# Kernel tuning notes

Hardware: AMD Instinct MI355X
Metric: run time of the kernel (lower is better)

## Reference

```python
import jax, jax.numpy as jnp
import numpy as np

NEG_SLOPE = 0.01  # torch F.leaky_relu default


def _gat_stack(x, W, a1w, a1b, a2w, a2b):
    """One GAT stack over all heads.
    x: (B, N, F_in); W: (H, F_in, d); a1w/a2w: (H, d); a1b/a2b: (H,)
    returns (B, N, H*d) -- heads concatenated in order along last dim.
    """
    # 1x1 conv1d (no bias) == per-node linear projection
    fts = jnp.einsum('bnf,hfd->hbnd', x, W)                      # (H,B,N,d)
    f1 = jnp.einsum('hbnd,hd->hbn', fts, a1w) + a1b[:, None, None]
    f2 = jnp.einsum('hbnd,hd->hbn', fts, a2w) + a2b[:, None, None]
    # logits[h,b,i,j] = f1[h,b,i] + f2[h,b,j]  (f_1.permute + f_2 broadcast)
    logits = f1[:, :, :, None] + f2[:, :, None, :]               # (H,B,N,N)
    coefs = jax.nn.softmax(jax.nn.leaky_relu(logits, NEG_SLOPE), axis=-1)
    vals = jnp.einsum('hbnm,hbmd->hbnd', coefs, fts)             # bmm aggregation
    ret = jax.nn.elu(vals + fts)                                 # residual-within-head + ELU activation
    B, N = x.shape[0], x.shape[1]
    return jnp.transpose(ret, (1, 2, 0, 3)).reshape(B, N, -1)    # cat(heads, dim=-1)


def setup_inputs() -> dict:
    key = jax.random.key(0)
    ks = jax.random.split(key, 7)
    B, N, F_in, H, d = 32, 512, 128, 8, 64
    hidden = H * d  # 512
    s = 0.05
    return {
        'x':   jax.random.normal(ks[0], (B, N, F_in), jnp.float32),
        'W0':  jax.random.normal(ks[1], (H, F_in, d), jnp.float32) * s,
        'W1':  jax.random.normal(ks[2], (H, hidden, d), jnp.float32) * s,
        'a1w': jax.random.normal(ks[3], (2, H, d), jnp.float32) * s,
        'a1b': jax.random.normal(ks[4], (2, H), jnp.float32) * s,
        'a2w': jax.random.normal(ks[5], (2, H, d), jnp.float32) * s,
        'a2b': jax.random.normal(ks[6], (2, H), jnp.float32) * s,
    }


def reference(x, W0, W1, a1w, a1b, a2w, a2b):
    # stack 0: input dim = num_random_sample
    h = _gat_stack(x, W0, a1w[0], a1b[0], a2w[0], a2b[0])
    # stack 1: input dim = hidden_dim
    out = _gat_stack(h, W1, a1w[1], a1b[1], a2w[1], a2b[1])
    return out
```

## Files before the change

kernel.cpp:

```cpp
#include <hip/hip_runtime.h>
#include <hip/hip_bf16.h>
#include <stdint.h>

typedef __attribute__((ext_vector_type(8))) short short8;
typedef __attribute__((ext_vector_type(4))) float f32x4;

#define L2E 1.44269504f

__device__ __forceinline__ short f2bf(float f) {
    unsigned u = __builtin_bit_cast(unsigned, f);
    return (short)((u + 0x8000u) >> 16);
}
__device__ __forceinline__ float bf2f(short s) {
    unsigned u = ((unsigned)(unsigned short)s) << 16;
    return __builtin_bit_cast(float, u);
}

__global__ void wtrans_kernel(const float* __restrict__ W0, const float* __restrict__ W1,
                              short* __restrict__ BT0, short* __restrict__ BT1) {
    int idx = blockIdx.x * 256 + threadIdx.x;
    if (idx < 8 * 128 * 64) {
        int h = idx >> 13;
        int k = (idx >> 6) & 127;
        int dd = idx & 63;
        BT0[(h * 64 + dd) * 128 + k] = f2bf(W0[idx]);
    } else {
        int j = idx - 8 * 128 * 64;
        int h = j >> 15;
        int k = (j >> 6) & 511;
        int dd = j & 63;
        BT1[(h * 64 + dd) * 512 + k] = f2bf(W1[j]);
    }
}

template <typename AT>
__global__ __launch_bounds__(256, 2)
void gemm_kernel(const AT* __restrict__ A, const short* __restrict__ BT,
                 short* __restrict__ fts, int K) {
    __shared__ __align__(16) short As[128 * 40];
    __shared__ __align__(16) short Bs[128 * 40];

    const int tid  = threadIdx.x;
    const int lane = tid & 63;
    const int w    = tid >> 6;
    const int wr   = w >> 1, wc = w & 1;
    const int quad = lane >> 4, l15 = lane & 15;
    const int m0   = blockIdx.y * 128;
    const int n0   = blockIdx.x * 128;

    f32x4 acc[4][4];
    for (int i = 0; i < 4; ++i)
        for (int j = 0; j < 4; ++j) { f32x4 z = {0.f, 0.f, 0.f, 0.f}; acc[i][j] = z; }

    const int nkb = K >> 5;
    for (int kb = 0; kb < nkb; ++kb) {
        __syncthreads();
        if constexpr (sizeof(AT) == 4) {
            for (int i = 0; i < 4; ++i) {
                int id  = tid + i * 256;
                int row = id >> 3, kc = id & 7;
                float4 v = *(const float4*)((const float*)A + (size_t)(m0 + row) * K + kb * 32 + kc * 4);
                ushort4 p;
                p.x = (unsigned short)f2bf(v.x);
                p.y = (unsigned short)f2bf(v.y);
                p.z = (unsigned short)f2bf(v.z);
                p.w = (unsigned short)f2bf(v.w);
                *(ushort4*)(As + row * 40 + kc * 4) = p;
            }
        } else {
            for (int i = 0; i < 2; ++i) {
                int id  = tid + i * 256;
                int row = id >> 2, kc = id & 3;
                uint4 va = *(const uint4*)((const short*)A + (size_t)(m0 + row) * K + kb * 32 + kc * 8);
                *(uint4*)(As + row * 40 + kc * 8) = va;
            }
        }
        for (int i = 0; i < 2; ++i) {
            int id  = tid + i * 256;
            int row = id >> 2, kc = id & 3;
            uint4 vb = *(const uint4*)(BT + (size_t)(n0 + row) * K + kb * 32 + kc * 8);
            *(uint4*)(Bs + row * 40 + kc * 8) = vb;
        }
        __syncthreads();
        short8 af[4], bf[4];
        for (int mf = 0; mf < 4; ++mf)
            af[mf] = *(const short8*)(As + (wr * 64 + mf * 16 + l15) * 40 + quad * 8);
        for (int nf = 0; nf < 4; ++nf)
            bf[nf] = *(const short8*)(Bs + (wc * 64 + nf * 16 + l15) * 40 + quad * 8);
        for (int mf = 0; mf < 4; ++mf)
            for (int nf = 0; nf < 4; ++nf)
                acc[mf][nf] = __builtin_amdgcn_mfma_f32_16x16x32_bf16(af[mf], bf[nf], acc[mf][nf], 0, 0, 0);
    }

    for (int nf = 0; nf < 4; ++nf) {
        int col = n0 + wc * 64 + nf * 16 + l15;
        int h = col >> 6, dd = col & 63;
        for (int mf = 0; mf < 4; ++mf) {
            int m = m0 + wr * 64 + mf * 16 + quad * 4;
            int b = m >> 9, n = m & 511;
            ushort4 pk;
            pk.x = (unsigned short)f2bf(acc[mf][nf][0]);
            pk.y = (unsigned short)f2bf(acc[mf][nf][1]);
            pk.z = (unsigned short)f2bf(acc[mf][nf][2]);
            pk.w = (unsigned short)f2bf(acc[mf][nf][3]);
            *(ushort4*)(fts + (size_t)((h * 32 + b) * 64 + dd) * 512 + n) = pk;
        }
    }
}

template <typename OutT>
__global__ __launch_bounds__(256, 4)
void attn_kernel(const short* __restrict__ fts,
                 const float* __restrict__ a1w, const float* __restrict__ a1b,
                 const float* __restrict__ a2w, const float* __restrict__ a2b,
                 OutT* __restrict__ out) {
    __shared__ __align__(16) short fts_s[64 * 256];
    __shared__ float f1_s[128];
    __shared__ __align__(16) float f2_s[256];
    __shared__ __align__(16) float p2_s[256];
    __shared__ __align__(16) float q2_s[256];

    const int tid  = threadIdx.x;
    const int lane = tid & 63, w = tid >> 6;
    const int quad = lane >> 4, l15 = lane & 15;
    const int bx   = blockIdx.x;
    const int h    = bx >> 7;
    const int b    = (bx >> 2) & 31;
    const int quarter = bx & 3;
    const int r0   = quarter * 128;
    const int c0   = quarter >> 1;
    const size_t fbase = (size_t)((h * 32 + b) * 64) * 512;

    f32x4 acc[2][4];
    for (int i = 0; i < 2; ++i)
        for (int j = 0; j < 4; ++j) { f32x4 z = {0.f, 0.f, 0.f, 0.f}; acc[i][j] = z; }
    float Lp[2] = {0.f, 0.f};
    float f1r[2], P1r[2], Q1r[2];

    const float a1bf = a1b[h], a2bf = a2b[h];

    for (int ci = 0; ci < 2; ++ci) {
        const int c = (ci == 0) ? c0 : 1 - c0;
        __syncthreads();
        for (int i = 0; i < 8; ++i) {
            int id = tid + i * 256;
            int dd = id >> 5, nc = id & 31;
            uint4 v = *(const uint4*)(fts + fbase + dd * 512 + c * 256 + nc * 8);
            *(uint4*)(fts_s + dd * 256 + ((nc ^ (dd & 7)) << 3)) = v;
        }
        __syncthreads();
        {
            int j = tid;
            float s1 = 0.f, s2 = 0.f;
            for (int dd = 0; dd < 64; ++dd) {
                float v = bf2f(fts_s[dd * 256 + (((j >> 3) ^ (dd & 7)) << 3) + (j & 7)]);
                s1 += v * a1w[h * 64 + dd];
                s2 += v * a2w[h * 64 + dd];
            }
            float f2 = s2 + a2bf;
            f2_s[j] = f2;
            p2_s[j] = __builtin_amdgcn_exp2f(f2 * L2E);
            q2_s[j] = __builtin_amdgcn_exp2f(f2 * (0.01f * L2E));
            if (ci == 0) {
                int lo = r0 & 255;
                if (((unsigned)(j - lo)) < 128u) f1_s[j - lo] = s1 + a1bf;
            }
        }
        __syncthreads();
        if (ci == 0) {
            for (int rt = 0; rt < 2; ++rt) {
                float f1 = f1_s[w * 32 + rt * 16 + l15];
                f1r[rt] = f1;
                P1r[rt] = __builtin_amdgcn_exp2f(f1 * L2E);
                Q1r[rt] = __builtin_amdgcn_exp2f(f1 * (0.01f * L2E));
            }
        }
        for (int jb = 0; jb < 8; ++jb) {
            short8 bfr[4];
            for (int nf = 0; nf < 4; ++nf) {
                int col = nf * 16 + l15;
                bfr[nf] = *(const short8*)(fts_s + col * 256 + (((jb * 4 + quad) ^ (col & 7)) << 3));
            }
            int o = jb * 32 + quad * 8;
            f32x4 fa = *(const f32x4*)(f2_s + o), fb = *(const f32x4*)(f2_s + o + 4);
            f32x4 pa = *(const f32x4*)(p2_s + o), pb = *(const f32x4*)(p2_s + o + 4);
            f32x4 qa = *(const f32x4*)(q2_s + o), qb = *(const f32x4*)(q2_s + o + 4);
            float f2v[8] = {fa[0], fa[1], fa[2], fa[3], fb[0], fb[1], fb[2], fb[3]};
            float p2v[8] = {pa[0], pa[1], pa[2], pa[3], pb[0], pb[1], pb[2], pb[3]};
            float q2v[8] = {qa[0], qa[1], qa[2], qa[3], qb[0], qb[1], qb[2], qb[3]};

            for (int rt = 0; rt < 2; ++rt) {
                short8 ef;
                float lsum = 0.f;
                for (int t = 0; t < 8; ++t) {
                    float s = f1r[rt] + f2v[t];
                    float e = (s < 0.f) ? (Q1r[rt] * q2v[t]) : (P1r[rt] * p2v[t]);
                    lsum += e;
                    ef[t] = f2bf(e);
                }
                Lp[rt] += lsum;
                for (int nf = 0; nf < 4; ++nf)
                    acc[rt][nf] = __builtin_amdgcn_mfma_f32_16x16x32_bf16(ef, bfr[nf], acc[rt][nf], 0, 0, 0);
            }
        }
    }

    for (int rt = 0; rt < 2; ++rt) {
        float Lf = Lp[rt];
        Lf += __shfl_xor(Lf, 16, 64);
        Lf += __shfl_xor(Lf, 32, 64);
        float rinv[4];
        for (int r = 0; r < 4; ++r) {
            float Lr = __shfl(Lf, quad * 4 + r, 64);
            rinv[r] = __builtin_amdgcn_rcpf(Lr);
        }
        int i0 = r0 + w * 32 + rt * 16 + quad * 4;
        for (int nf = 0; nf < 4; ++nf) {
            int col = nf * 16 + l15;
            ushort4 res = *(const ushort4*)(fts + fbase + col * 512 + i0);
            unsigned short rr[4] = {res.x, res.y, res.z, res.w};
            for (int r = 0; r < 4; ++r) {
                float val = acc[rt][nf][r] * rinv[r] + bf2f((short)rr[r]);
                if (val < 0.f) val = __builtin_amdgcn_exp2f(val * L2E) - 1.f;
                size_t oidx = (size_t)(b * 512 + i0 + r) * 512 + h * 64 + col;
                if constexpr (sizeof(OutT) == 4) out[oidx] = val;
                else                             out[oidx] = f2bf(val);
            }
        }
    }
}

extern "C" void kernel_launch(void* const* d_in, const int* in_sizes, int n_in,
                              void* d_out, int out_size, void* d_ws, size_t ws_size,
                              hipStream_t stream) {
    const float* x   = (const float*)d_in[0];
    const float* W0  = (const float*)d_in[1];
    const float* W1  = (const float*)d_in[2];
    const float* a1w = (const float*)d_in[3];
    const float* a1b = (const float*)d_in[4];
    const float* a2w = (const float*)d_in[5];
    const float* a2b = (const float*)d_in[6];
    float* out = (float*)d_out;

    char* ws = (char*)d_ws;
    short* BT0 = (short*)(ws);
    short* BT1 = (short*)(ws + 131072);
    short* fts = (short*)(ws + 655360);
    short* hbuf = (short*)d_out;

    wtrans_kernel<<<1280, 256, 0, stream>>>(W0, W1, BT0, BT1);

    gemm_kernel<float><<<dim3(4, 128), 256, 0, stream>>>(x, BT0, fts, 128);
    attn_kernel<short><<<1024, 256, 0, stream>>>(fts, a1w, a1b, a2w, a2b, hbuf);

    gemm_kernel<short><<<dim3(4, 128), 256, 0, stream>>>(hbuf, BT1, fts, 512);
    attn_kernel<float><<<1024, 256, 0, stream>>>(fts, a1w + 512, a1b + 8, a2w + 512, a2b + 8, out);
}
```

Measured before the change: 176.9 us.

## Fuse attention logit projections into GEMM epilogue and use direct global-to-LDS loads

The GEMM epilogue now reduces the accumulator tiles against a1w/a2w with lane shuffles and writes f1, f2 and their exponentials to a workspace buffer. The attention kernel reads these values instead of recomputing the 64-wide dot products and exps for every block, which removes an extra LDS pass and a sync. GEMM and attention tile loads switch to global_load_lds with XOR-swizzled unpadded LDS layouts. The cost is extra global traffic for the six per-node float arrays and more epilogue work in the GEMM.

```diff
diff --git a/kernel.cpp b/kernel.cpp
--- a/kernel.cpp
+++ b/kernel.cpp
@@ -6,6 +6,7 @@
 typedef __attribute__((ext_vector_type(4))) float f32x4;
 
 #define L2E 1.44269504f
+#define FN  131072
 
 __device__ __forceinline__ short f2bf(float f) {
     unsigned u = __builtin_bit_cast(unsigned, f);
@@ -14,6 +15,12 @@
 __device__ __forceinline__ float bf2f(short s) {
     unsigned u = ((unsigned)(unsigned short)s) << 16;
     return __builtin_bit_cast(float, u);
+}
+
+__device__ __forceinline__ void gld16(void* l, const void* g) {
+    __builtin_amdgcn_global_load_lds(
+        (const __attribute__((address_space(1))) unsigned*)g,
+        (__attribute__((address_space(3))) unsigned*)l, 16, 0, 0);
 }
 
 __global__ void wtrans_kernel(const float* __restrict__ W0, const float* __restrict__ W1,
@@ -36,9 +43,12 @@
 template <typename AT>
 __global__ __launch_bounds__(256, 2)
 void gemm_kernel(const AT* __restrict__ A, const short* __restrict__ BT,
-                 short* __restrict__ fts, int K) {
-    __shared__ __align__(16) short As[128 * 40];
-    __shared__ __align__(16) short Bs[128 * 40];
+                 short* __restrict__ fts, int K,
+                 const float* __restrict__ a1w, const float* __restrict__ a1b,
+                 const float* __restrict__ a2w, const float* __restrict__ a2b,
+                 float* __restrict__ fbuf) {
+    __shared__ __align__(16) short As[128 * 32];
+    __shared__ __align__(16) short Bs[128 * 32];
 
     const int tid  = threadIdx.x;
     const int lane = tid & 63;
@@ -48,6 +58,10 @@
     const int m0   = blockIdx.y * 128;
     const int n0   = blockIdx.x * 128;
 
+    const int rl   = lane >> 2;
+    const int cpos = lane & 3;
+    const int kcl  = cpos ^ ((rl >> 1) & 3);
+
     f32x4 acc[4][4];
     for (int i = 0; i < 4; ++i)
         for (int j = 0; j < 4; ++j) { f32x4 z = {0.f, 0.f, 0.f, 0.f}; acc[i][j] = z; }
@@ -58,35 +72,39 @@
         if constexpr (sizeof(AT) == 4) {
             for (int i = 0; i < 4; ++i) {
                 int id  = tid + i * 256;
-                int row = id >> 3, kc = id & 7;
-                float4 v = *(const float4*)((const float*)A + (size_t)(m0 + row) * K + kb * 32 + kc * 4);
+                int row = id >> 3, q = id & 7;
+                int kc = q >> 1, half = q & 1;
+                float4 v = *(const float4*)((const float*)A + (size_t)(m0 + row) * K + kb * 32 + q * 4);
                 ushort4 p;
                 p.x = (unsigned short)f2bf(v.x);
                 p.y = (unsigned short)f2bf(v.y);
                 p.z = (unsigned short)f2bf(v.z);
                 p.w = (unsigned short)f2bf(v.w);
-                *(ushort4*)(As + row * 40 + kc * 4) = p;
+                int swz = kc ^ ((row >> 1) & 3);
+                *(ushort4*)(As + row * 32 + swz * 8 + half * 4) = p;
             }
         } else {
             for (int i = 0; i < 2; ++i) {
-                int id  = tid + i * 256;
-                int row = id >> 2, kc = id & 3;
-                uint4 va = *(const uint4*)((const short*)A + (size_t)(m0 + row) * K + kb * 32 + kc * 8);
-                *(uint4*)(As + row * 40 + kc * 8) = va;
+                int row = w * 32 + i * 16 + rl;
+                gld16(As + (w * 32 + i * 16) * 32,
+                      (const short*)A + (size_t)(m0 + row) * K + kb * 32 + kcl * 8);
             }
         }
         for (int i = 0; i < 2; ++i) {
-            int id  = tid + i * 256;
-            int row = id >> 2, kc = id & 3;
-            uint4 vb = *(const uint4*)(BT + (size_t)(n0 + row) * K + kb * 32 + kc * 8);
-            *(uint4*)(Bs + row * 40 + kc * 8) = vb;
+            int row = w * 32 + i * 16 + rl;
+            gld16(Bs + (w * 32 + i * 16) * 32,
+                  BT + (size_t)(n0 + row) * K + kb * 32 + kcl * 8);
         }
         __syncthreads();
         short8 af[4], bf[4];
-        for (int mf = 0; mf < 4; ++mf)
-            af[mf] = *(const short8*)(As + (wr * 64 + mf * 16 + l15) * 40 + quad * 8);
-        for (int nf = 0; nf < 4; ++nf)
-            bf[nf] = *(const short8*)(Bs + (wc * 64 + nf * 16 + l15) * 40 + quad * 8);
+        for (int mf = 0; mf < 4; ++mf) {
+            int row = wr * 64 + mf * 16 + l15;
+            af[mf] = *(const short8*)(As + row * 32 + ((quad ^ ((row >> 1) & 3)) << 3));
+        }
+        for (int nf = 0; nf < 4; ++nf) {
+            int row = wc * 64 + nf * 16 + l15;
+            bf[nf] = *(const short8*)(Bs + row * 32 + ((quad ^ ((row >> 1) & 3)) << 3));
+        }
         for (int mf = 0; mf < 4; ++mf)
             for (int nf = 0; nf < 4; ++nf)
                 acc[mf][nf] = __builtin_amdgcn_mfma_f32_16x16x32_bf16(af[mf], bf[nf], acc[mf][nf], 0, 0, 0);
@@ -106,16 +124,53 @@
             *(ushort4*)(fts + (size_t)((h * 32 + b) * 64 + dd) * 512 + n) = pk;
         }
     }
+
+    {
+        const int head = (n0 >> 6) + wc;
+        float w1[4], w2[4];
+        for (int nf = 0; nf < 4; ++nf) {
+            w1[nf] = a1w[head * 64 + nf * 16 + l15];
+            w2[nf] = a2w[head * 64 + nf * 16 + l15];
+        }
+        const float b1 = a1b[head], b2 = a2b[head];
+        const int rsel = l15 & 3;
+        for (int mf = 0; mf < 4; ++mf) {
+            float g1[4], g2[4];
+            for (int r = 0; r < 4; ++r) {
+                float s1 = 0.f, s2 = 0.f;
+                for (int nf = 0; nf < 4; ++nf) {
+                    s1 += acc[mf][nf][r] * w1[nf];
+                    s2 += acc[mf][nf][r] * w2[nf];
+                }
+                for (int m = 1; m < 16; m <<= 1) {
+                    s1 += __shfl_xor(s1, m, 64);
+                    s2 += __shfl_xor(s2, m, 64);
+                }
+                g1[r] = s1; g2[r] = s2;
+            }
+            float v1 = rsel == 0 ? g1[0] : rsel == 1 ? g1[1] : rsel == 2 ? g1[2] : g1[3];
+            float v2 = rsel == 0 ? g2[0] : rsel == 1 ? g2[1] : rsel == 2 ? g2[2] : g2[3];
+            if (l15 < 4) {
+                int m = m0 + wr * 64 + mf * 16 + quad * 4 + rsel;
+                int b = m >> 9, i = m & 511;
+                int fi = (head * 32 + b) * 512 + i;
+                float f1 = v1 + b1, f2 = v2 + b2;
+                fbuf[0 * FN + fi] = f1;
+                fbuf[1 * FN + fi] = __builtin_amdgcn_exp2f(f1 * L2E);
+                fbuf[2 * FN + fi] = __builtin_amdgcn_exp2f(f1 * (0.01f * L2E));
+                fbuf[3 * FN + fi] = f2;
+                fbuf[4 * FN + fi] = __builtin_amdgcn_exp2f(f2 * L2E);
+                fbuf[5 * FN + fi] = __builtin_amdgcn_exp2f(f2 * (0.01f * L2E));
+            }
+        }
+    }
 }
 
 template <typename OutT>
 __global__ __launch_bounds__(256, 4)
-void attn_kernel(const short* __restrict__ fts,
-                 const float* __restrict__ a1w, const float* __restrict__ a1b,
-                 const float* __restrict__ a2w, const float* __restrict__ a2b,
+void attn_kernel(const short* __restrict__ fts, const float* __restrict__ fbuf,
                  OutT* __restrict__ out) {
     __shared__ __align__(16) short fts_s[64 * 256];
-    __shared__ float f1_s[128];
     __shared__ __align__(16) float f2_s[256];
     __shared__ __align__(16) float p2_s[256];
     __shared__ __align__(16) float q2_s[256];
@@ -128,53 +183,38 @@
     const int b    = (bx >> 2) & 31;
     const int quarter = bx & 3;
     const int r0   = quarter * 128;
-    const int c0   = quarter >> 1;
     const size_t fbase = (size_t)((h * 32 + b) * 64) * 512;
+    const int fidx = (h * 32 + b) * 512;
 
     f32x4 acc[2][4];
     for (int i = 0; i < 2; ++i)
         for (int j = 0; j < 4; ++j) { f32x4 z = {0.f, 0.f, 0.f, 0.f}; acc[i][j] = z; }
     float Lp[2] = {0.f, 0.f};
+
     float f1r[2], P1r[2], Q1r[2];
-
-    const float a1bf = a1b[h], a2bf = a2b[h];
-
-    for (int ci = 0; ci < 2; ++ci) {
-        const int c = (ci == 0) ? c0 : 1 - c0;
+    for (int rt = 0; rt < 2; ++rt) {
+        int i = fidx + r0 + w * 32 + rt * 16 + l15;
+        f1r[rt] = fbuf[i];
+        P1r[rt] = fbuf[1 * FN + i];
+        Q1r[rt] = fbuf[2 * FN + i];
+    }
+
+    for (int c = 0; c < 2; ++c) {
         __syncthreads();
         for (int i = 0; i < 8; ++i) {
             int id = tid + i * 256;
             int dd = id >> 5, nc = id & 31;
-            uint4 v = *(const uint4*)(fts + fbase + dd * 512 + c * 256 + nc * 8);
-            *(uint4*)(fts_s + dd * 256 + ((nc ^ (dd & 7)) << 3)) = v;
+            gld16(fts_s + (i * 256 + w * 64) * 8,
+                  fts + fbase + dd * 512 + c * 256 + ((nc ^ (dd & 7)) << 3));
+        }
+        {
+            int j = fidx + c * 256 + tid;
+            f2_s[tid] = fbuf[3 * FN + j];
+            p2_s[tid] = fbuf[4 * FN + j];
+            q2_s[tid] = fbuf[5 * FN + j];
         }
         __syncthreads();
-        {
-            int j = tid;
-            float s1 = 0.f, s2 = 0.f;
-            for (int dd = 0; dd < 64; ++dd) {
-                float v = bf2f(fts_s[dd * 256 + (((j >> 3) ^ (dd & 7)) << 3) + (j & 7)]);
-                s1 += v * a1w[h * 64 + dd];
-                s2 += v * a2w[h * 64 + dd];
-            }
-            float f2 = s2 + a2bf;
-            f2_s[j] = f2;
-            p2_s[j] = __builtin_amdgcn_exp2f(f2 * L2E);
-            q2_s[j] = __builtin_amdgcn_exp2f(f2 * (0.01f * L2E));
-            if (ci == 0) {
-                int lo = r0 & 255;
-                if (((unsigned)(j - lo)) < 128u) f1_s[j - lo] = s1 + a1bf;
-            }
-        }
-        __syncthreads();
-        if (ci == 0) {
-            for (int rt = 0; rt < 2; ++rt) {
-                float f1 = f1_s[w * 32 + rt * 16 + l15];
-                f1r[rt] = f1;
-                P1r[rt] = __builtin_amdgcn_exp2f(f1 * L2E);
-                Q1r[rt] = __builtin_amdgcn_exp2f(f1 * (0.01f * L2E));
-            }
-        }
+
         for (int jb = 0; jb < 8; ++jb) {
             short8 bfr[4];
             for (int nf = 0; nf < 4; ++nf) {
@@ -243,16 +283,19 @@
     float* out = (float*)d_out;
 
     char* ws = (char*)d_ws;
-    short* BT0 = (short*)(ws);
-    short* BT1 = (short*)(ws + 131072);
-    short* fts = (short*)(ws + 655360);
+    short* BT0  = (short*)(ws);
+    short* BT1  = (short*)(ws + 131072);
+    float* fbuf = (float*)(ws + 655360);
+    short* fts  = (short*)(ws + 3801088);
     short* hbuf = (short*)d_out;
 
     wtrans_kernel<<<1280, 256, 0, stream>>>(W0, W1, BT0, BT1);
 
-    gemm_kernel<float><<<dim3(4, 128), 256, 0, stream>>>(x, BT0, fts, 128);
-    attn_kernel<short><<<1024, 256, 0, stream>>>(fts, a1w, a1b, a2w, a2b, hbuf);
-
-    gemm_kernel<short><<<dim3(4, 128), 256, 0, stream>>>(hbuf, BT1, fts, 512);
-    attn_kernel<float><<<1024, 256, 0, stream>>>(fts, a1w + 512, a1b + 8, a2w + 512, a2b + 8, out);
-}
+    gemm_kernel<float><<<dim3(4, 128), 256, 0, stream>>>(x, BT0, fts, 128,
+                                                         a1w, a1b, a2w, a2b, fbuf);
+    attn_kernel<short><<<1024, 256, 0, stream>>>(fts, fbuf, hbuf);
+
+    gemm_kernel<short><<<dim3(4, 128), 256, 0, stream>>>(hbuf, BT1, fts, 512,
+                                                         a1w + 512, a1b + 8, a2w + 512, a2b + 8, fbuf);
+    attn_kernel<float><<<1024, 256, 0, stream>>>(fts, fbuf, out);
+}
```

Result: faster. 167.1 us (-5.5%).
